# Performance work log

Hardware: AMD Instinct MI355X
Metric: run time of the kernel (lower is better)

Reference implementation:

```python
import jax, jax.numpy as jnp
import numpy as np


def setup_inputs() -> dict:
    key = jax.random.key(0)
    k1, k2 = jax.random.split(key)
    B, H, N, C = 8, 8, 2048, 64
    x = jax.random.normal(k1, (B, H, N, C), dtype=jnp.float32)
    # torch nn.Linear(dim, 3*dim) weight layout: [3C, C]
    W_qkv = jax.random.normal(k2, (3 * C, C), dtype=jnp.float32) * (C ** -0.5)
    return {"x": x, "W_qkv": W_qkv}


def reference(x, W_qkv):
    B, H, N, C = x.shape
    scale = C ** -0.5
    # fused qkv projection: x @ W^T, then split
    qkv = jnp.einsum('bhnc,dc->bhnd', x, W_qkv)  # [B,H,N,3C]
    q, k, v = jnp.split(qkv, 3, axis=-1)
    # full N x N score matrix (matches the naive original)
    attn = jnp.einsum('bhnc,bhmc->bhnm', q, k) * scale
    attn = jax.nn.softmax(attn, axis=-1)
    out = jnp.einsum('bhnm,bhmc->bhnc', attn, v)  # [B,H,N,C]
    # head-mixing shuffle: reshape(B,H,N,H,C//H).transpose(1,3).reshape(B,H,N,C)
    out = out.reshape(B, H, N, H, C // H)
    out = out.transpose(0, 3, 2, 1, 4)
    return out.reshape(B, H, N, C)
```

## Files before the change

kernel.cpp:

```cpp
#include <hip/hip_runtime.h>
#include <math.h>

#define BH    64
#define NSEQ  2048
#define CDIM  64
#define WSTR  72
#define PTILES 4

typedef unsigned short ushort_t;
typedef __attribute__((ext_vector_type(8))) short short8;
typedef __attribute__((ext_vector_type(4))) float float4v;

__device__ __forceinline__ ushort_t f32_to_bf16_rne(float x) {
  unsigned int u = __float_as_uint(x);
  u += 0x7fffu + ((u >> 16) & 1u);
  return (ushort_t)(u >> 16);
}

__device__ __forceinline__ unsigned int cvtpk(float a, float b) {
  unsigned int r;
  asm("v_cvt_pk_bf16_f32 %0, %1, %2" : "=v"(r) : "v"(a), "v"(b));
  return r;
}

__device__ __forceinline__ void glds16(const ushort_t* g, ushort_t* l) {
  __builtin_amdgcn_global_load_lds(
      (const __attribute__((address_space(1))) void*)g,
      (__attribute__((address_space(3))) void*)l, 16, 0, 0);
}

__global__ __launch_bounds__(256) void qkv_proj_mfma(
    const float* __restrict__ x, const float* __restrict__ w,
    ushort_t* __restrict__ q, ushort_t* __restrict__ k,
    ushort_t* __restrict__ vt) {
  __shared__ ushort_t Wb[192 * WSTR];
  __shared__ ushort_t Sg[128 * 64];
  const int t = threadIdx.x;
  const int lane = t & 63, wv = t >> 6;
  const int quad = lane >> 4, l16 = lane & 15;
  const long rb0 = (long)blockIdx.x * (128 * PTILES);

  for (int u = t; u < 1536; u += 256) {
    const int d = u >> 3, o8 = (u & 7) * 8;
    const float sc = (d < 64) ? 0.1803368801111244f : 1.0f;
    const float4 f0 = *reinterpret_cast<const float4*>(w + d * 64 + o8);
    const float4 f1 = *reinterpret_cast<const float4*>(w + d * 64 + o8 + 4);
    ushort_t tmp[8] __attribute__((aligned(16)));
    tmp[0] = f32_to_bf16_rne(f0.x * sc); tmp[1] = f32_to_bf16_rne(f0.y * sc);
    tmp[2] = f32_to_bf16_rne(f0.z * sc); tmp[3] = f32_to_bf16_rne(f0.w * sc);
    tmp[4] = f32_to_bf16_rne(f1.x * sc); tmp[5] = f32_to_bf16_rne(f1.y * sc);
    tmp[6] = f32_to_bf16_rne(f1.z * sc); tmp[7] = f32_to_bf16_rne(f1.w * sc);
    *reinterpret_cast<uint4*>(&Wb[d * WSTR + o8]) = *reinterpret_cast<const uint4*>(tmp);
  }

  short8 xf[2][2];
#pragma unroll
  for (int tm = 0; tm < 2; ++tm)
#pragma unroll
    for (int kb = 0; kb < 2; ++kb) {
      const float* xp = x + (rb0 + wv * 32 + tm * 16 + l16) * 64 + kb * 32 + quad * 8;
      const float4 f0 = *reinterpret_cast<const float4*>(xp);
      const float4 f1 = *reinterpret_cast<const float4*>(xp + 4);
      ushort_t tmp[8] __attribute__((aligned(16)));
      tmp[0] = f32_to_bf16_rne(f0.x); tmp[1] = f32_to_bf16_rne(f0.y);
      tmp[2] = f32_to_bf16_rne(f0.z); tmp[3] = f32_to_bf16_rne(f0.w);
      tmp[4] = f32_to_bf16_rne(f1.x); tmp[5] = f32_to_bf16_rne(f1.y);
      tmp[6] = f32_to_bf16_rne(f1.z); tmp[7] = f32_to_bf16_rne(f1.w);
      xf[tm][kb] = *reinterpret_cast<const short8*>(tmp);
    }
  __syncthreads();

#pragma unroll
  for (int tile = 0; tile < PTILES; ++tile) {
    const long rowbase = rb0 + (long)tile * 128;
    const int head  = (int)(rowbase >> 11);
    const int nbase = (int)(rowbase & 2047);

    float4v aqk[8][2];
    float4v av[2][4];
#pragma unroll
    for (int nt = 0; nt < 8; ++nt)
#pragma unroll
      for (int tm = 0; tm < 2; ++tm)
#pragma unroll
        for (int r = 0; r < 4; ++r) aqk[nt][tm][r] = 0.f;
#pragma unroll
    for (int tm = 0; tm < 2; ++tm)
#pragma unroll
      for (int nt = 0; nt < 4; ++nt)
#pragma unroll
        for (int r = 0; r < 4; ++r) av[tm][nt][r] = 0.f;

#pragma unroll
    for (int kb = 0; kb < 2; ++kb) {
#pragma unroll
      for (int nt = 0; nt < 8; ++nt) {
        const short8 wf = *reinterpret_cast<const short8*>(
            &Wb[(nt * 16 + l16) * WSTR + kb * 32 + quad * 8]);
        aqk[nt][0] = __builtin_amdgcn_mfma_f32_16x16x32_bf16(wf, xf[0][kb], aqk[nt][0], 0, 0, 0);
        aqk[nt][1] = __builtin_amdgcn_mfma_f32_16x16x32_bf16(wf, xf[1][kb], aqk[nt][1], 0, 0, 0);
      }
#pragma unroll
      for (int nt = 0; nt < 4; ++nt) {
        const short8 wfv = *reinterpret_cast<const short8*>(
            &Wb[((128 + nt * 16) + l16) * WSTR + kb * 32 + quad * 8]);
        av[0][nt] = __builtin_amdgcn_mfma_f32_16x16x32_bf16(xf[0][kb], wfv, av[0][nt], 0, 0, 0);
        av[1][nt] = __builtin_amdgcn_mfma_f32_16x16x32_bf16(xf[1][kb], wfv, av[1][nt], 0, 0, 0);
      }
    }

    float4 nx[8];
    if (tile < PTILES - 1) {
#pragma unroll
      for (int tm = 0; tm < 2; ++tm)
#pragma unroll
        for (int kb = 0; kb < 2; ++kb) {
          const float* xp = x + (rowbase + 128 + wv * 32 + tm * 16 + l16) * 64 + kb * 32 + quad * 8;
          nx[(tm * 2 + kb) * 2]     = *reinterpret_cast<const float4*>(xp);
          nx[(tm * 2 + kb) * 2 + 1] = *reinterpret_cast<const float4*>(xp + 4);
        }
    }

    __syncthreads();

#pragma unroll
    for (int tm = 0; tm < 2; ++tm) {
      const int row = wv * 32 + tm * 16 + l16;
#pragma unroll
      for (int nt = 0; nt < 4; ++nt) {
        const int dchunk = nt * 2 + (quad >> 1);
        uint2 pk;
        pk.x = cvtpk(aqk[nt][tm][0], aqk[nt][tm][1]);
        pk.y = cvtpk(aqk[nt][tm][2], aqk[nt][tm][3]);
        *reinterpret_cast<uint2*>(
            &Sg[row * 64 + ((dchunk ^ (row & 7)) * 8) + (quad & 1) * 4]) = pk;
      }
    }
    __syncthreads();
#pragma unroll
    for (int i = 0; i < 4; ++i) {
      const int g = i * 256 + t;
      const int row = g >> 3, ch = g & 7;
      const uint4 v = *reinterpret_cast<const uint4*>(
          &Sg[row * 64 + ((ch ^ (row & 7)) * 8)]);
      *reinterpret_cast<uint4*>(q + (rowbase + row) * 64 + ch * 8) = v;
    }
    __syncthreads();

#pragma unroll
    for (int tm = 0; tm < 2; ++tm) {
      const int row = wv * 32 + tm * 16 + l16;
#pragma unroll
      for (int nt = 4; nt < 8; ++nt) {
        const int dchunk = (nt - 4) * 2 + (quad >> 1);
        uint2 pk;
        pk.x = cvtpk(aqk[nt][tm][0], aqk[nt][tm][1]);
        pk.y = cvtpk(aqk[nt][tm][2], aqk[nt][tm][3]);
        *reinterpret_cast<uint2*>(
            &Sg[row * 64 + ((dchunk ^ (row & 7)) * 8) + (quad & 1) * 4]) = pk;
      }
    }
    __syncthreads();
#pragma unroll
    for (int i = 0; i < 4; ++i) {
      const int g = i * 256 + t;
      const int row = g >> 3, ch = g & 7;
      const uint4 v = *reinterpret_cast<const uint4*>(
          &Sg[row * 64 + ((ch ^ (row & 7)) * 8)]);
      *reinterpret_cast<uint4*>(k + (rowbase + row) * 64 + ch * 8) = v;
    }
    __syncthreads();

#pragma unroll
    for (int tm = 0; tm < 2; ++tm)
#pragma unroll
      for (int nt = 0; nt < 4; ++nt) {
        const int c = nt * 16 + l16;
        const int nchunk = wv * 4 + tm * 2 + (quad >> 1);
        uint2 pk;
        pk.x = cvtpk(av[tm][nt][0], av[tm][nt][1]);
        pk.y = cvtpk(av[tm][nt][2], av[tm][nt][3]);
        *reinterpret_cast<uint2*>(
            &Sg[c * 128 + ((nchunk ^ (c & 15)) * 8) + (quad & 1) * 4]) = pk;
      }
    __syncthreads();
#pragma unroll
    for (int i = 0; i < 4; ++i) {
      const int g = i * 256 + t;
      const int c = g >> 4, ch = g & 15;
      const uint4 v = *reinterpret_cast<const uint4*>(
          &Sg[c * 128 + ((ch ^ (c & 15)) * 8)]);
      *reinterpret_cast<uint4*>(vt + (long)head * (64 * 2048) + (long)c * 2048 +
                                nbase + ch * 8) = v;
    }

    if (tile < PTILES - 1) {
#pragma unroll
      for (int tm = 0; tm < 2; ++tm)
#pragma unroll
        for (int kb = 0; kb < 2; ++kb) {
          const float4 f0 = nx[(tm * 2 + kb) * 2];
          const float4 f1 = nx[(tm * 2 + kb) * 2 + 1];
          ushort_t tmp[8] __attribute__((aligned(16)));
          tmp[0] = f32_to_bf16_rne(f0.x); tmp[1] = f32_to_bf16_rne(f0.y);
          tmp[2] = f32_to_bf16_rne(f0.z); tmp[3] = f32_to_bf16_rne(f0.w);
          tmp[4] = f32_to_bf16_rne(f1.x); tmp[5] = f32_to_bf16_rne(f1.y);
          tmp[6] = f32_to_bf16_rne(f1.z); tmp[7] = f32_to_bf16_rne(f1.w);
          xf[tm][kb] = *reinterpret_cast<const short8*>(tmp);
        }
    }
  }
}

__global__ __launch_bounds__(512, 4) void flash_attn_mfma(
    const ushort_t* __restrict__ q, const ushort_t* __restrict__ k,
    const ushort_t* __restrict__ vt, float* __restrict__ out) {
  __shared__ ushort_t Ks2[2][32 * 64];
  __shared__ ushort_t Vs2[2][64 * 32];
  __shared__ ushort_t Ps[256 * 32];
  const int t = threadIdx.x;
  const int lane = t & 63, w = t >> 6;
  const int quad = lane >> 4, l16 = lane & 15;
  const int id = blockIdx.x;
  const int qt = id >> 6;
  const int bh = ((id & 7) << 3) | ((id >> 3) & 7);
  const long hoff = (long)bh * NSEQ * CDIM;
  const ushort_t* qp  = q  + hoff + (long)qt * 256 * CDIM;
  const ushort_t* kp  = k  + hoff;
  const ushort_t* vtp = vt + hoff;

  short8 qf[2][2];
#pragma unroll
  for (int tm = 0; tm < 2; ++tm)
#pragma unroll
    for (int kb = 0; kb < 2; ++kb)
      qf[tm][kb] = *reinterpret_cast<const short8*>(
          qp + (w * 32 + tm * 16 + l16) * 64 + kb * 32 + quad * 8);

  float4v O[4][2];
  float rs[2];
  rs[0] = 0.f; rs[1] = 0.f;
#pragma unroll
  for (int ct = 0; ct < 4; ++ct)
#pragma unroll
    for (int tm = 0; tm < 2; ++tm)
#pragma unroll
      for (int r = 0; r < 4; ++r) O[ct][tm][r] = 0.f;

  const int ws = w & 3;
  const bool isK = (w < 4);
  const int krow = ws * 8 + (lane >> 3);
  const int kchk = (lane & 7) ^ (lane >> 3);
  const int kdst = ws * 8 * 64;
  const int vrow = ws * 16 + (lane >> 2);
  const int vchk = (lane & 3) ^ ((lane >> 3) & 3);
  const int vdst = ws * 16 * 32;
  const int pswz = (l16 >> 1) & 3;

  if (isK) glds16(kp + (long)krow * 64 + kchk * 8, &Ks2[0][kdst]);
  else     glds16(vtp + (long)vrow * 2048 + vchk * 8, &Vs2[0][vdst]);

  for (int tile = 0; tile < NSEQ / 32; ++tile) {
    const int cur = tile & 1;
    __syncthreads();
    if (tile < NSEQ / 32 - 1) {
      const long nxt = tile + 1;
      if (isK) glds16(kp + (nxt * 32 + krow) * 64 + kchk * 8, &Ks2[1 - cur][kdst]);
      else     glds16(vtp + (long)vrow * 2048 + nxt * 32 + vchk * 8, &Vs2[1 - cur][vdst]);
    }

    float4v s[2][2];
#pragma unroll
    for (int nt = 0; nt < 2; ++nt)
#pragma unroll
      for (int tm = 0; tm < 2; ++tm)
#pragma unroll
        for (int r = 0; r < 4; ++r) s[nt][tm][r] = 0.f;

#pragma unroll
    for (int kb = 0; kb < 2; ++kb) {
      short8 kf[2];
#pragma unroll
      for (int nt = 0; nt < 2; ++nt)
        kf[nt] = *reinterpret_cast<const short8*>(
            &Ks2[cur][(nt * 16 + l16) * 64 + (((kb * 4 + quad) ^ (l16 & 7)) * 8)]);
#pragma unroll
      for (int nt = 0; nt < 2; ++nt)
#pragma unroll
        for (int tm = 0; tm < 2; ++tm)
          s[nt][tm] = __builtin_amdgcn_mfma_f32_16x16x32_bf16(
              kf[nt], qf[tm][kb], s[nt][tm], 0, 0, 0);
    }

#pragma unroll
    for (int tm = 0; tm < 2; ++tm)
#pragma unroll
      for (int nt = 0; nt < 2; ++nt) {
        const float p0 = __builtin_amdgcn_exp2f(s[nt][tm][0]);
        const float p1 = __builtin_amdgcn_exp2f(s[nt][tm][1]);
        const float p2 = __builtin_amdgcn_exp2f(s[nt][tm][2]);
        const float p3 = __builtin_amdgcn_exp2f(s[nt][tm][3]);
        rs[tm] += (p0 + p1) + (p2 + p3);
        uint2 pk;
        pk.x = cvtpk(p0, p1);
        pk.y = cvtpk(p2, p3);
        *reinterpret_cast<uint2*>(
            &Ps[(w * 32 + tm * 16 + l16) * 32 +
                (((nt * 2 + (quad >> 1)) ^ pswz) * 8) + (quad & 1) * 4]) = pk;
      }

    {
      short8 pf[2], vf[4];
#pragma unroll
      for (int tm = 0; tm < 2; ++tm)
        pf[tm] = *reinterpret_cast<const short8*>(
            &Ps[(w * 32 + tm * 16 + l16) * 32 + ((quad ^ pswz) * 8)]);
#pragma unroll
      for (int ct = 0; ct < 4; ++ct)
        vf[ct] = *reinterpret_cast<const short8*>(
            &Vs2[cur][(ct * 16 + l16) * 32 + ((quad ^ pswz) * 8)]);
#pragma unroll
      for (int ct = 0; ct < 4; ++ct)
#pragma unroll
        for (int tm = 0; tm < 2; ++tm)
          O[ct][tm] = __builtin_amdgcn_mfma_f32_16x16x32_bf16(
              vf[ct], pf[tm], O[ct][tm], 0, 0, 0);
    }
  }

  const int bi = bh >> 3, h = bh & 7;
  float inv[2];
#pragma unroll
  for (int tm = 0; tm < 2; ++tm) {
    float l = rs[tm];
    l += __shfl_xor(l, 16, 64);
    l += __shfl_xor(l, 32, 64);
    inv[tm] = 1.f / l;
  }
#pragma unroll
  for (int ct = 0; ct < 4; ++ct)
#pragma unroll
    for (int tm = 0; tm < 2; ++tm) {
      const int n = qt * 256 + w * 32 + tm * 16 + l16;
      const int h2 = ct * 2 + (quad >> 1);
      const int c2b = (quad & 1) * 4;
      float4 v4;
      v4.x = O[ct][tm][0] * inv[tm]; v4.y = O[ct][tm][1] * inv[tm];
      v4.z = O[ct][tm][2] * inv[tm]; v4.w = O[ct][tm][3] * inv[tm];
      *reinterpret_cast<float4*>(
          &out[(((long)(bi * 8 + h2)) * NSEQ + n) * 64 + h * 8 + c2b]) = v4;
    }
}

extern "C" void kernel_launch(void* const* d_in, const int* in_sizes, int n_in,
                              void* d_out, int out_size, void* d_ws, size_t ws_size,
                              hipStream_t stream) {
  (void)in_sizes; (void)n_in; (void)out_size; (void)ws_size;
  const float* x = (const float*)d_in[0];
  const float* w = (const float*)d_in[1];
  float* out = (float*)d_out;

  ushort_t* qws  = (ushort_t*)d_ws;
  ushort_t* kws  = qws + (size_t)BH * NSEQ * CDIM;
  ushort_t* vtws = kws + (size_t)BH * NSEQ * CDIM;

  qkv_proj_mfma<<<(BH * NSEQ) / (128 * PTILES), 256, 0, stream>>>(x, w, qws, kws, vtws);
  flash_attn_mfma<<<512, 512, 0, stream>>>(qws, kws, vtws, out);
}
```

Before: 167.2 us.

## Process two KV tiles per barrier with four-stage K/V buffers

The KV loop now handles a pair of 32-row tiles per iteration, with four K and V shared-memory stages and two P buffers. This halves the number of __syncthreads barriers, and each prefetch now loads two tiles ahead. The cost is doubled shared-memory use per block (about 64KB), which caps how many blocks fit on a CU. With this grid size that cap may not bind.

```diff
diff --git a/kernel.cpp b/kernel.cpp
--- a/kernel.cpp
+++ b/kernel.cpp
@@ -215,9 +215,9 @@
 __global__ __launch_bounds__(512, 4) void flash_attn_mfma(
     const ushort_t* __restrict__ q, const ushort_t* __restrict__ k,
     const ushort_t* __restrict__ vt, float* __restrict__ out) {
-  __shared__ ushort_t Ks2[2][32 * 64];
-  __shared__ ushort_t Vs2[2][64 * 32];
-  __shared__ ushort_t Ps[256 * 32];
+  __shared__ ushort_t Ks2[4][32 * 64];
+  __shared__ ushort_t Vs2[4][64 * 32];
+  __shared__ ushort_t Ps[2][256 * 32];
   const int t = threadIdx.x;
   const int lane = t & 63, w = t >> 6;
   const int quad = lane >> 4, l16 = lane & 15;
@@ -257,74 +257,90 @@
   const int vdst = ws * 16 * 32;
   const int pswz = (l16 >> 1) & 3;
 
-  if (isK) glds16(kp + (long)krow * 64 + kchk * 8, &Ks2[0][kdst]);
-  else     glds16(vtp + (long)vrow * 2048 + vchk * 8, &Vs2[0][vdst]);
-
-  for (int tile = 0; tile < NSEQ / 32; ++tile) {
-    const int cur = tile & 1;
-    __syncthreads();
-    if (tile < NSEQ / 32 - 1) {
-      const long nxt = tile + 1;
-      if (isK) glds16(kp + (nxt * 32 + krow) * 64 + kchk * 8, &Ks2[1 - cur][kdst]);
-      else     glds16(vtp + (long)vrow * 2048 + nxt * 32 + vchk * 8, &Vs2[1 - cur][vdst]);
-    }
-
-    float4v s[2][2];
-#pragma unroll
-    for (int nt = 0; nt < 2; ++nt)
+  if (isK) {
+    glds16(kp + (long)krow * 64 + kchk * 8, &Ks2[0][kdst]);
+    glds16(kp + (long)(32 + krow) * 64 + kchk * 8, &Ks2[1][kdst]);
+  } else {
+    glds16(vtp + (long)vrow * 2048 + vchk * 8, &Vs2[0][vdst]);
+    glds16(vtp + (long)vrow * 2048 + 32 + vchk * 8, &Vs2[1][vdst]);
+  }
+
+  for (int pair = 0; pair < NSEQ / 64; ++pair) {
+    const int base = (pair & 1) << 1;
+    __syncthreads();
+    if (pair < NSEQ / 64 - 1) {
+      const int nb = base ^ 2;
+      const long t2 = (long)pair * 2 + 2;
+      if (isK) {
+        glds16(kp + ((t2 * 32) + krow) * 64 + kchk * 8, &Ks2[nb][kdst]);
+        glds16(kp + (((t2 + 1) * 32) + krow) * 64 + kchk * 8, &Ks2[nb + 1][kdst]);
+      } else {
+        glds16(vtp + (long)vrow * 2048 + t2 * 32 + vchk * 8, &Vs2[nb][vdst]);
+        glds16(vtp + (long)vrow * 2048 + (t2 + 1) * 32 + vchk * 8, &Vs2[nb + 1][vdst]);
+      }
+    }
+
+#pragma unroll
+    for (int kk = 0; kk < 2; ++kk) {
+      const int cur = base + kk;
+
+      float4v s[2][2];
+#pragma unroll
+      for (int nt = 0; nt < 2; ++nt)
+#pragma unroll
+        for (int tm = 0; tm < 2; ++tm)
+#pragma unroll
+          for (int r = 0; r < 4; ++r) s[nt][tm][r] = 0.f;
+
+#pragma unroll
+      for (int kb = 0; kb < 2; ++kb) {
+        short8 kf[2];
+#pragma unroll
+        for (int nt = 0; nt < 2; ++nt)
+          kf[nt] = *reinterpret_cast<const short8*>(
+              &Ks2[cur][(nt * 16 + l16) * 64 + (((kb * 4 + quad) ^ (l16 & 7)) * 8)]);
+#pragma unroll
+        for (int nt = 0; nt < 2; ++nt)
+#pragma unroll
+          for (int tm = 0; tm < 2; ++tm)
+            s[nt][tm] = __builtin_amdgcn_mfma_f32_16x16x32_bf16(
+                kf[nt], qf[tm][kb], s[nt][tm], 0, 0, 0);
+      }
+
 #pragma unroll
       for (int tm = 0; tm < 2; ++tm)
 #pragma unroll
-        for (int r = 0; r < 4; ++r) s[nt][tm][r] = 0.f;
-
-#pragma unroll
-    for (int kb = 0; kb < 2; ++kb) {
-      short8 kf[2];
-#pragma unroll
-      for (int nt = 0; nt < 2; ++nt)
-        kf[nt] = *reinterpret_cast<const short8*>(
-            &Ks2[cur][(nt * 16 + l16) * 64 + (((kb * 4 + quad) ^ (l16 & 7)) * 8)]);
-#pragma unroll
-      for (int nt = 0; nt < 2; ++nt)
+        for (int nt = 0; nt < 2; ++nt) {
+          const float p0 = __builtin_amdgcn_exp2f(s[nt][tm][0]);
+          const float p1 = __builtin_amdgcn_exp2f(s[nt][tm][1]);
+          const float p2 = __builtin_amdgcn_exp2f(s[nt][tm][2]);
+          const float p3 = __builtin_amdgcn_exp2f(s[nt][tm][3]);
+          rs[tm] += (p0 + p1) + (p2 + p3);
+          uint2 pk;
+          pk.x = cvtpk(p0, p1);
+          pk.y = cvtpk(p2, p3);
+          *reinterpret_cast<uint2*>(
+              &Ps[kk][(w * 32 + tm * 16 + l16) * 32 +
+                  (((nt * 2 + (quad >> 1)) ^ pswz) * 8) + (quad & 1) * 4]) = pk;
+        }
+
+      {
+        short8 pf[2], vf[4];
 #pragma unroll
         for (int tm = 0; tm < 2; ++tm)
-          s[nt][tm] = __builtin_amdgcn_mfma_f32_16x16x32_bf16(
-              kf[nt], qf[tm][kb], s[nt][tm], 0, 0, 0);
-    }
-
-#pragma unroll
-    for (int tm = 0; tm < 2; ++tm)
-#pragma unroll
-      for (int nt = 0; nt < 2; ++nt) {
-        const float p0 = __builtin_amdgcn_exp2f(s[nt][tm][0]);
-        const float p1 = __builtin_amdgcn_exp2f(s[nt][tm][1]);
-        const float p2 = __builtin_amdgcn_exp2f(s[nt][tm][2]);
-        const float p3 = __builtin_amdgcn_exp2f(s[nt][tm][3]);
-        rs[tm] += (p0 + p1) + (p2 + p3);
-        uint2 pk;
-        pk.x = cvtpk(p0, p1);
-        pk.y = cvtpk(p2, p3);
-        *reinterpret_cast<uint2*>(
-            &Ps[(w * 32 + tm * 16 + l16) * 32 +
-                (((nt * 2 + (quad >> 1)) ^ pswz) * 8) + (quad & 1) * 4]) = pk;
-      }
-
-    {
-      short8 pf[2], vf[4];
-#pragma unroll
-      for (int tm = 0; tm < 2; ++tm)
-        pf[tm] = *reinterpret_cast<const short8*>(
-            &Ps[(w * 32 + tm * 16 + l16) * 32 + ((quad ^ pswz) * 8)]);
-#pragma unroll
-      for (int ct = 0; ct < 4; ++ct)
-        vf[ct] = *reinterpret_cast<const short8*>(
-            &Vs2[cur][(ct * 16 + l16) * 32 + ((quad ^ pswz) * 8)]);
-#pragma unroll
-      for (int ct = 0; ct < 4; ++ct)
-#pragma unroll
-        for (int tm = 0; tm < 2; ++tm)
-          O[ct][tm] = __builtin_amdgcn_mfma_f32_16x16x32_bf16(
-              vf[ct], pf[tm], O[ct][tm], 0, 0, 0);
+          pf[tm] = *reinterpret_cast<const short8*>(
+              &Ps[kk][(w * 32 + tm * 16 + l16) * 32 + ((quad ^ pswz) * 8)]);
+#pragma unroll
+        for (int ct = 0; ct < 4; ++ct)
+          vf[ct] = *reinterpret_cast<const short8*>(
+              &Vs2[cur][(ct * 16 + l16) * 32 + ((quad ^ pswz) * 8)]);
+#pragma unroll
+        for (int ct = 0; ct < 4; ++ct)
+#pragma unroll
+          for (int tm = 0; tm < 2; ++tm)
+            O[ct][tm] = __builtin_amdgcn_mfma_f32_16x16x32_bf16(
+                vf[ct], pf[tm], O[ct][tm], 0, 0, 0);
+      }
     }
   }
 
```

Result: no change. 165.4 us (-1.1%).
